# Optimization experiments

Measured on AMD Instinct MI355X. Metric: run time of the kernel, lower is better.

Reference implementation:

```python
import jax, jax.numpy as jnp
import numpy as np

MARGIN = 0.2
ALPHA = 2.0
BETA = 1.5
ANGLE_THRESHOLD = 30.0
EPS_PD = 1e-6   # F.pairwise_distance eps
EPS_CS = 1e-8   # F.cosine_similarity eps
NEG_INF = -1e30
POS_INF = 1e30


def setup_inputs() -> dict:
    key = jax.random.key(0)
    k1, k2, k3 = jax.random.split(key, 3)
    B, F, A = 4096, 512, 3
    features = jax.random.normal(k1, (B, F), dtype=jnp.float32)
    labels = jax.random.randint(k2, (B,), 0, 256)
    angles = jax.random.uniform(k3, (B, A), dtype=jnp.float32) * 90.0  # degrees
    features_orig = jax.random.normal(jax.random.fold_in(key, 7), (B, F), dtype=jnp.float32)
    return {"features": features, "labels": labels, "angles": angles, "features_orig": features_orig}


def _cosine_sim_matrix(f):
    norms = jnp.linalg.norm(f, axis=1)
    denom = jnp.maximum(norms[:, None] * norms[None, :], EPS_CS)
    return (f @ f.T) / denom


def _forward(features, labels, angles, features_orig):
    B = features.shape[0]
    idx = jnp.arange(B)
    # pairwise angle distances [B,B] (torch.cdist p=2)
    adist = jnp.sqrt(jnp.sum((angles[:, None, :] - angles[None, :, :]) ** 2, axis=-1))
    same = labels[:, None] == labels[None, :]
    same = same & ~jnp.eye(B, dtype=bool)          # exclude self
    diff = labels[:, None] != labels[None, :]
    has_pos = same.any(axis=1)
    has_neg = diff.any(axis=1)
    valid = has_pos & has_neg
    # hardest positive: same label, largest angle difference
    pos_idx = jnp.argmax(jnp.where(same, adist, NEG_INF), axis=1)
    # hardest negative: among diff-label within angle threshold, most similar feature;
    # else diff-label with smallest angle difference
    sim = _cosine_sim_matrix(features)
    similar = diff & (adist < ANGLE_THRESHOLD)
    sim_any = similar.any(axis=1)
    neg_idx_hard = jnp.argmax(jnp.where(similar, sim, NEG_INF), axis=1)
    neg_idx_far = jnp.argmin(jnp.where(diff, adist, POS_INF), axis=1)
    neg_idx = jnp.where(sim_any, neg_idx_hard, neg_idx_far)
    # triplet distances (F.pairwise_distance adds eps to the diff)
    a = features
    p = features[pos_idx]
    n = features[neg_idx]
    pos_d = jnp.linalg.norm(a - p + EPS_PD, axis=1)
    neg_d = jnp.linalg.norm(a - n + EPS_PD, axis=1)
    # angle-based weights (non-differentiable, matches .item() in torch)
    pa = adist[idx, pos_idx]
    na = adist[idx, neg_idx]
    w = jnp.where(pa > 45.0, ALPHA, 1.0) * jnp.where(na < 15.0, BETA, 1.0)
    basic = jax.nn.relu(pos_d - neg_d + MARGIN)
    vmask = valid.astype(features.dtype)
    cnt = jnp.maximum(vmask.sum(), 1.0)
    triplet_loss = jnp.sum(w * basic * vmask) / cnt
    # reconstruction term
    num = jnp.sum(features * features_orig, axis=1)
    den = jnp.maximum(jnp.linalg.norm(features, axis=1) * jnp.linalg.norm(features_orig, axis=1), EPS_CS)
    recon = 1.0 - jnp.mean(num / den)
    return triplet_loss + 0.1 * recon


def reference(features, labels, angles, features_orig):
    return _forward(features, labels, angles, features_orig)
```

## Files before the change

### kernel.cpp

```cpp
#include <hip/hip_runtime.h>
#include <math.h>

#define BN 4096
#define FD 512
#define TT 128
#define TJ 64
#define BK 64
#define NJT (BN / TT)
#define NPAIR (NJT * (NJT + 1) / 2)
#define NBLK (NPAIR * 2)
#define NPC 128

typedef __attribute__((ext_vector_type(8))) __bf16 bf16x8;
typedef __attribute__((ext_vector_type(4))) float floatx4;
typedef unsigned long long u64;

__device__ __forceinline__ float wred_sum(float v) {
#pragma unroll
  for (int m = 1; m < 64; m <<= 1) v += __shfl_xor(v, m, 64);
  return v;
}

__device__ __forceinline__ float dot4(float4 a, float4 b) {
  return a.x * b.x + a.y * b.y + a.z * b.z + a.w * b.w;
}

__device__ __forceinline__ unsigned short f2bf(float x) {
  unsigned u = __float_as_uint(x);
  u += 0x7fffu + ((u >> 16) & 1u);
  return (unsigned short)(u >> 16);
}

__device__ __forceinline__ void load16(const void* g, void* l) {
  __builtin_amdgcn_global_load_lds(
      (const __attribute__((address_space(1))) unsigned int*)g,
      (__attribute__((address_space(3))) unsigned int*)l, 16, 0, 0);
}

__device__ __forceinline__ unsigned ford(float v) {
  unsigned u = __float_as_uint(v);
  return u ^ (((unsigned)((int)u >> 31)) | 0x80000000u);
}

template <int N>
__device__ __forceinline__ int rori(int x) {
  return __builtin_amdgcn_update_dpp(0, x, 0x120 | N, 0xf, 0xf, true);
}
template <int N>
__device__ __forceinline__ u64 ror16_u64(u64 k) {
  unsigned lo = (unsigned)rori<N>((int)(unsigned)k);
  unsigned hi = (unsigned)rori<N>((int)(unsigned)(k >> 32));
  return ((u64)hi << 32) | lo;
}
__device__ __forceinline__ u64 red16_max_u64(u64 k) {
  u64 o;
  o = ror16_u64<1>(k); k = o > k ? o : k;
  o = ror16_u64<2>(k); k = o > k ? o : k;
  o = ror16_u64<4>(k); k = o > k ? o : k;
  o = ror16_u64<8>(k); k = o > k ? o : k;
  return k;
}

__device__ __forceinline__ u64 sx64(u64 v, int m) {
  unsigned lo = (unsigned)__shfl_xor((int)(unsigned)v, m, 64);
  unsigned hi = (unsigned)__shfl_xor((int)(unsigned)(v >> 32), m, 64);
  return ((u64)hi << 32) | lo;
}

__global__ __launch_bounds__(256) void k_prep(const float* __restrict__ f,
                                              const float* __restrict__ fo,
                                              const float* __restrict__ angles,
                                              unsigned short* __restrict__ gb,
                                              float* __restrict__ rowr,
                                              float* __restrict__ ax,
                                              float* __restrict__ ay,
                                              float* __restrict__ az) {
  const int i = blockIdx.x * 4 + (threadIdx.x >> 6);
  const int lane = threadIdx.x & 63;
  const int t = blockIdx.x * 256 + threadIdx.x;
  if (t < BN) {
    ax[t] = angles[t * 3 + 0];
    ay[t] = angles[t * 3 + 1];
    az[t] = angles[t * 3 + 2];
  }
  const float4* fr = (const float4*)(f + (size_t)i * FD);
  const float4* orr = (const float4*)(fo + (size_t)i * FD);
  float4 x0 = fr[lane], x1 = fr[lane + 64];
  float4 y0 = orr[lane], y1 = orr[lane + 64];
  float sff = dot4(x0, x0) + dot4(x1, x1);
  float sfo = dot4(x0, y0) + dot4(x1, y1);
  float soo = dot4(y0, y0) + dot4(y1, y1);
  sff = wred_sum(sff);
  sfo = wred_sum(sfo);
  soo = wred_sum(soo);
  float nf = sqrtf(sff);
  float inv = 1.0f / nf;
  ushort4* gr = (ushort4*)(gb + (size_t)i * FD);
  ushort4 s0, s1;
  s0.x = f2bf(x0.x * inv); s0.y = f2bf(x0.y * inv);
  s0.z = f2bf(x0.z * inv); s0.w = f2bf(x0.w * inv);
  s1.x = f2bf(x1.x * inv); s1.y = f2bf(x1.y * inv);
  s1.z = f2bf(x1.z * inv); s1.w = f2bf(x1.w * inv);
  gr[lane] = s0;
  gr[lane + 64] = s1;
  if (lane == 0) {
    rowr[i] = sfo / fmaxf(nf * sqrtf(soo), 1e-8f);
  }
}

__global__ __launch_bounds__(256, 4) void k_sim(const unsigned short* __restrict__ gb,
                                                const int* __restrict__ labels,
                                                const float* __restrict__ ax,
                                                const float* __restrict__ ay,
                                                const float* __restrict__ az,
                                                u64* __restrict__ pkey) {
  __shared__ unsigned short As[TT * BK];
  __shared__ unsigned short Bs[TJ * BK];
  const int h = blockIdx.x & 1;
  int a = 0, rem = blockIdx.x >> 1;
#pragma unroll 1
  while (rem >= NJT - a) { rem -= NJT - a; a++; }
  const int b = a + rem;
  const int i0 = a * TT;
  const int j0 = b * TT + h * TJ;

  const int tid = threadIdx.x;
  const int w = tid >> 6;
  const int lane = tid & 63;

  floatx4 acc[2][4];
#pragma unroll
  for (int u = 0; u < 2; u++)
#pragma unroll
    for (int v = 0; v < 4; v++) acc[u][v] = (floatx4){0.f, 0.f, 0.f, 0.f};

  const int rp = tid >> 3;
  const int q8 = ((tid & 7) ^ (rp & 7)) * 8;
  const unsigned short* gA[4];
  const unsigned short* gB[2];
  unsigned short* lA[4];
  unsigned short* lB[2];
#pragma unroll
  for (int c = 0; c < 4; c++) {
    gA[c] = gb + (size_t)(i0 + rp + 32 * c) * FD + q8;
    lA[c] = As + (tid + 256 * c) * 8;
  }
#pragma unroll
  for (int c = 0; c < 2; c++) {
    gB[c] = gb + (size_t)(j0 + rp + 32 * c) * FD + q8;
    lB[c] = Bs + (tid + 256 * c) * 8;
  }

  const int m = lane & 15;
  const int arow = w * 32 + m;
  const int brow = m;
  const int g4 = lane >> 4;
  const int l7 = lane & 7;
  const int koff0 = (g4 ^ l7) * 8;
  const int koff1 = ((4 + g4) ^ l7) * 8;

  for (int kc = 0; kc < FD; kc += BK) {
#pragma unroll
    for (int c = 0; c < 4; c++) load16(gA[c] + kc, lA[c]);
#pragma unroll
    for (int c = 0; c < 2; c++) load16(gB[c] + kc, lB[c]);
    __syncthreads();
    bf16x8 af[2], bf[4];
#pragma unroll
    for (int u = 0; u < 2; u++)
      af[u] = *(const bf16x8*)(As + (arow + u * 16) * BK + koff0);
#pragma unroll
    for (int v = 0; v < 4; v++)
      bf[v] = *(const bf16x8*)(Bs + (brow + v * 16) * BK + koff0);
#pragma unroll
    for (int u = 0; u < 2; u++)
#pragma unroll
      for (int v = 0; v < 4; v++)
        acc[u][v] = __builtin_amdgcn_mfma_f32_16x16x32_bf16(af[u], bf[v], acc[u][v], 0, 0, 0);
#pragma unroll
    for (int u = 0; u < 2; u++)
      af[u] = *(const bf16x8*)(As + (arow + u * 16) * BK + koff1);
#pragma unroll
    for (int v = 0; v < 4; v++)
      bf[v] = *(const bf16x8*)(Bs + (brow + v * 16) * BK + koff1);
#pragma unroll
    for (int u = 0; u < 2; u++)
#pragma unroll
      for (int v = 0; v < 4; v++)
        acc[u][v] = __builtin_amdgcn_mfma_f32_16x16x32_bf16(af[u], bf[v], acc[u][v], 0, 0, 0);
    __syncthreads();
  }

  const int quad = lane >> 4;
  const int cx = lane & 15;
  int jc[4], lj[4];
  float jx[4], jy[4], jz[4];
#pragma unroll
  for (int v = 0; v < 4; v++) {
    jc[v] = j0 + v * 16 + cx;
    lj[v] = labels[jc[v]];
    jx[v] = ax[jc[v]];
    jy[v] = ay[jc[v]];
    jz[v] = az[jc[v]];
  }
  const size_t rbase = (size_t)(64 + 2 * b + h) * BN;
  u64 ckey[4] = {0, 0, 0, 0};
#pragma unroll
  for (int u = 0; u < 2; u++) {
#pragma unroll
    for (int reg = 0; reg < 4; reg++) {
      int i = i0 + w * 32 + u * 16 + quad * 4 + reg;
      int li = labels[i];
      float a0 = ax[i], a1 = ay[i], a2 = az[i];
      u64 rkey = 0;
      unsigned ni = (unsigned)(~i);
#pragma unroll
      for (int v = 0; v < 4; v++) {
        float d0 = a0 - jx[v];
        float d1 = a1 - jy[v];
        float d2 = a2 - jz[v];
        float dd = d0 * d0 + d1 * d1 + d2 * d2;
        bool ok = (li != lj[v]) && (dd < 900.0f);
        u64 vh = (u64)ford(acc[u][v][reg]) << 32;
        u64 candR = vh | (unsigned)(~jc[v]);
        if (ok && candR > rkey) rkey = candR;
        u64 candC = vh | ni;
        if (ok && candC > ckey[v]) ckey[v] = candC;
      }
      rkey = red16_max_u64(rkey);
      if (cx == 0) pkey[rbase + i] = rkey;
    }
  }
  if (a != b) {
    const size_t cbase = (size_t)(4 * a + w) * BN;
#pragma unroll
    for (int v = 0; v < 4; v++) {
      u64 k = ckey[v];
      u64 o = sx64(k, 16); if (o > k) k = o;
      o = sx64(k, 32); if (o > k) k = o;
      if (quad == 0) pkey[cbase + jc[v]] = k;
    }
  }
}

__global__ __launch_bounds__(256) void k_final(const float* __restrict__ f,
                                               const int* __restrict__ labels,
                                               const float* __restrict__ ax,
                                               const float* __restrict__ ay,
                                               const float* __restrict__ az,
                                               const u64* __restrict__ pkey,
                                               float* __restrict__ rowc,
                                               float* __restrict__ rowv) {
  const int i = blockIdx.x * 4 + (threadIdx.x >> 6);
  const int lane = threadIdx.x & 63;
  const int li = labels[i];
  const float a0 = ax[i], a1 = ay[i], a2 = az[i];

  u64 keyP = 0;
  u64 keyN = ~0ull;
  const float4* ax4 = (const float4*)ax;
  const float4* ay4 = (const float4*)ay;
  const float4* az4 = (const float4*)az;
  const int4* lb4 = (const int4*)labels;
#pragma unroll
  for (int it = 0; it < 16; it++) {
    int bb = it * 64 + lane;
    float4 X = ax4[bb], Y = ay4[bb], Z = az4[bb];
    int4 L = lb4[bb];
    int jb = bb * 4;
#pragma unroll
    for (int s = 0; s < 4; s++) {
      float xx = s == 0 ? X.x : s == 1 ? X.y : s == 2 ? X.z : X.w;
      float yy = s == 0 ? Y.x : s == 1 ? Y.y : s == 2 ? Y.z : Y.w;
      float zz = s == 0 ? Z.x : s == 1 ? Z.y : s == 2 ? Z.z : Z.w;
      int ll = s == 0 ? L.x : s == 1 ? L.y : s == 2 ? L.z : L.w;
      int j = jb + s;
      float d0 = a0 - xx, d1 = a1 - yy, d2 = a2 - zz;
      float dd = d0 * d0 + d1 * d1 + d2 * d2;
      if (ll == li) {
        u64 kp = ((u64)__float_as_uint(dd) << 32) | (unsigned)(~j);
        if (j != i && kp > keyP) keyP = kp;
      } else {
        u64 kn = ((u64)__float_as_uint(dd) << 32) | (unsigned)j;
        if (kn < keyN) keyN = kn;
      }
    }
  }
  const int t = i >> 7;
  u64 s0 = (lane < 4 * t) ? pkey[(size_t)lane * BN + i] : 0;
  u64 s1 = (lane >= 2 * t) ? pkey[(size_t)(64 + lane) * BN + i] : 0;
  u64 keyS = s0 > s1 ? s0 : s1;
#pragma unroll
  for (int off = 1; off < 64; off <<= 1) {
    u64 o = sx64(keyP, off);
    if (o > keyP) keyP = o;
    o = sx64(keyN, off);
    if (o < keyN) keyN = o;
    o = sx64(keyS, off);
    if (o > keyS) keyS = o;
  }
  bool hp = keyP != 0;
  bool hn = keyN != ~0ull;
  if (!(hp && hn)) {
    if (lane == 0) { rowc[i] = 0.0f; rowv[i] = 0.0f; }
    return;
  }
  bool sim_any = keyS != 0;
  int pos = (int)(~(unsigned)keyP);
  int neg = sim_any ? (int)(~(unsigned)keyS) : (int)(unsigned)keyN;

  const float4* fa = (const float4*)(f + (size_t)i * FD);
  const float4* fp = (const float4*)(f + (size_t)pos * FD);
  const float4* fn = (const float4*)(f + (size_t)neg * FD);
  float sp = 0.0f, sn = 0.0f;
#pragma unroll
  for (int t2 = 0; t2 < 2; t2++) {
    float4 xa = fa[lane + t2 * 64];
    float4 xp = fp[lane + t2 * 64];
    float4 xn = fn[lane + t2 * 64];
    float dp;
    dp = xa.x - xp.x + 1e-6f; sp += dp * dp;
    dp = xa.y - xp.y + 1e-6f; sp += dp * dp;
    dp = xa.z - xp.z + 1e-6f; sp += dp * dp;
    dp = xa.w - xp.w + 1e-6f; sp += dp * dp;
    dp = xa.x - xn.x + 1e-6f; sn += dp * dp;
    dp = xa.y - xn.y + 1e-6f; sn += dp * dp;
    dp = xa.z - xn.z + 1e-6f; sn += dp * dp;
    dp = xa.w - xn.w + 1e-6f; sn += dp * dp;
  }
  sp = wred_sum(sp);
  sn = wred_sum(sn);

  if (lane == 0) {
    float pos_d = sqrtf(sp);
    float neg_d = sqrtf(sn);
    float pa = sqrtf(__uint_as_float((unsigned)(keyP >> 32)));
    float n0 = a0 - ax[neg];
    float n1 = a1 - ay[neg];
    float n2 = a2 - az[neg];
    float na = sqrtf(n0 * n0 + n1 * n1 + n2 * n2);
    float w = (pa > 45.0f ? 2.0f : 1.0f) * (na < 15.0f ? 1.5f : 1.0f);
    float basic = fmaxf(pos_d - neg_d + 0.2f, 0.0f);
    rowc[i] = w * basic;
    rowv[i] = 1.0f;
  }
}

__global__ __launch_bounds__(1024) void k_out(const float* __restrict__ rowc,
                                              const float* __restrict__ rowv,
                                              const float* __restrict__ rowr,
                                              float* __restrict__ out) {
  __shared__ float sc[16], sv[16], sr[16];
  const int t = threadIdx.x;
  float c = 0.0f, v = 0.0f, r = 0.0f;
  for (int i = t; i < BN; i += 1024) {
    c += rowc[i];
    v += rowv[i];
    r += rowr[i];
  }
  c = wred_sum(c);
  v = wred_sum(v);
  r = wred_sum(r);
  const int wid = t >> 6;
  if ((t & 63) == 0) { sc[wid] = c; sv[wid] = v; sr[wid] = r; }
  __syncthreads();
  if (t == 0) {
    float C = 0.0f, V = 0.0f, R = 0.0f;
#pragma unroll
    for (int k = 0; k < 16; k++) { C += sc[k]; V += sv[k]; R += sr[k]; }
    float tri = C / fmaxf(V, 1.0f);
    float recon = 1.0f - R / (float)BN;
    out[0] = tri + 0.1f * recon;
  }
}

extern "C" void kernel_launch(void* const* d_in, const int* in_sizes, int n_in,
                              void* d_out, int out_size, void* d_ws, size_t ws_size,
                              hipStream_t stream) {
  const float* feat = (const float*)d_in[0];
  const int* labels = (const int*)d_in[1];
  const float* angles = (const float*)d_in[2];
  const float* forig = (const float*)d_in[3];
  float* out = (float*)d_out;

  char* ws = (char*)d_ws;
  unsigned short* gb = (unsigned short*)ws;
  size_t off = (size_t)BN * FD * sizeof(unsigned short);
  u64* pkey = (u64*)(ws + off);     off += (size_t)NPC * BN * 8;
  float* rowc = (float*)(ws + off); off += (size_t)BN * 4;
  float* rowv = (float*)(ws + off); off += (size_t)BN * 4;
  float* rowr = (float*)(ws + off); off += (size_t)BN * 4;
  float* ax = (float*)(ws + off);   off += (size_t)BN * 4;
  float* ay = (float*)(ws + off);   off += (size_t)BN * 4;
  float* az = (float*)(ws + off);   off += (size_t)BN * 4;

  k_prep<<<BN / 4, 256, 0, stream>>>(feat, forig, angles, gb, rowr, ax, ay, az);
  k_sim<<<NBLK, 256, 0, stream>>>(gb, labels, ax, ay, az, pkey);
  k_final<<<BN / 4, 256, 0, stream>>>(feat, labels, ax, ay, az, pkey, rowc, rowv);
  k_out<<<1, 1024, 0, stream>>>(rowc, rowv, rowr, out);
}
```

Measured before the change: 108.9 us.

## Fuse final reduction into k_final via atomics and remap k_sim block order

Result: slower. 129.3 us (+18.7%).

```diff
diff --git a/kernel.cpp b/kernel.cpp
--- a/kernel.cpp
+++ b/kernel.cpp
@@ -74,7 +74,15 @@
                                               float* __restrict__ rowr,
                                               float* __restrict__ ax,
                                               float* __restrict__ ay,
-                                              float* __restrict__ az) {
+                                              float* __restrict__ az,
+                                              float* __restrict__ acc,
+                                              unsigned* __restrict__ tick) {
+  if (blockIdx.x == 0 && threadIdx.x == 0) {
+    acc[0] = 0.0f;
+    acc[32] = 0.0f;
+    acc[64] = 0.0f;
+    tick[0] = 0u;
+  }
   const int i = blockIdx.x * 4 + (threadIdx.x >> 6);
   const int lane = threadIdx.x & 63;
   const int t = blockIdx.x * 256 + threadIdx.x;
@@ -116,8 +124,10 @@
                                                 u64* __restrict__ pkey) {
   __shared__ unsigned short As[TT * BK];
   __shared__ unsigned short Bs[TJ * BK];
-  const int h = blockIdx.x & 1;
-  int a = 0, rem = blockIdx.x >> 1;
+
+  const int bid = (blockIdx.x & 7) * (NBLK / 8) + (blockIdx.x >> 3);
+  const int h = bid & 1;
+  int a = 0, rem = bid >> 1;
 #pragma unroll 1
   while (rem >= NJT - a) { rem -= NJT - a; a++; }
   const int b = a + rem;
@@ -249,9 +259,12 @@
                                                const float* __restrict__ ay,
                                                const float* __restrict__ az,
                                                const u64* __restrict__ pkey,
-                                               float* __restrict__ rowc,
-                                               float* __restrict__ rowv) {
-  const int i = blockIdx.x * 4 + (threadIdx.x >> 6);
+                                               const float* __restrict__ rowr,
+                                               float* __restrict__ acc,
+                                               unsigned* __restrict__ tick,
+                                               float* __restrict__ out) {
+  const int wv = threadIdx.x >> 6;
+  const int i = blockIdx.x * 4 + wv;
   const int lane = threadIdx.x & 63;
   const int li = labels[i];
   const float a0 = ax[i], a1 = ay[i], a2 = az[i];
@@ -301,76 +314,72 @@
   }
   bool hp = keyP != 0;
   bool hn = keyN != ~0ull;
-  if (!(hp && hn)) {
-    if (lane == 0) { rowc[i] = 0.0f; rowv[i] = 0.0f; }
-    return;
-  }
-  bool sim_any = keyS != 0;
-  int pos = (int)(~(unsigned)keyP);
-  int neg = sim_any ? (int)(~(unsigned)keyS) : (int)(unsigned)keyN;
-
-  const float4* fa = (const float4*)(f + (size_t)i * FD);
-  const float4* fp = (const float4*)(f + (size_t)pos * FD);
-  const float4* fn = (const float4*)(f + (size_t)neg * FD);
-  float sp = 0.0f, sn = 0.0f;
-#pragma unroll
-  for (int t2 = 0; t2 < 2; t2++) {
-    float4 xa = fa[lane + t2 * 64];
-    float4 xp = fp[lane + t2 * 64];
-    float4 xn = fn[lane + t2 * 64];
-    float dp;
-    dp = xa.x - xp.x + 1e-6f; sp += dp * dp;
-    dp = xa.y - xp.y + 1e-6f; sp += dp * dp;
-    dp = xa.z - xp.z + 1e-6f; sp += dp * dp;
-    dp = xa.w - xp.w + 1e-6f; sp += dp * dp;
-    dp = xa.x - xn.x + 1e-6f; sn += dp * dp;
-    dp = xa.y - xn.y + 1e-6f; sn += dp * dp;
-    dp = xa.z - xn.z + 1e-6f; sn += dp * dp;
-    dp = xa.w - xn.w + 1e-6f; sn += dp * dp;
-  }
-  sp = wred_sum(sp);
-  sn = wred_sum(sn);
-
+  float ci = 0.0f, vi = 0.0f;
+  if (hp && hn) {
+    bool sim_any = keyS != 0;
+    int pos = (int)(~(unsigned)keyP);
+    int neg = sim_any ? (int)(~(unsigned)keyS) : (int)(unsigned)keyN;
+
+    const float4* fa = (const float4*)(f + (size_t)i * FD);
+    const float4* fp = (const float4*)(f + (size_t)pos * FD);
+    const float4* fn = (const float4*)(f + (size_t)neg * FD);
+    float sp = 0.0f, sn = 0.0f;
+#pragma unroll
+    for (int t2 = 0; t2 < 2; t2++) {
+      float4 xa = fa[lane + t2 * 64];
+      float4 xp = fp[lane + t2 * 64];
+      float4 xn = fn[lane + t2 * 64];
+      float dp;
+      dp = xa.x - xp.x + 1e-6f; sp += dp * dp;
+      dp = xa.y - xp.y + 1e-6f; sp += dp * dp;
+      dp = xa.z - xp.z + 1e-6f; sp += dp * dp;
+      dp = xa.w - xp.w + 1e-6f; sp += dp * dp;
+      dp = xa.x - xn.x + 1e-6f; sn += dp * dp;
+      dp = xa.y - xn.y + 1e-6f; sn += dp * dp;
+      dp = xa.z - xn.z + 1e-6f; sn += dp * dp;
+      dp = xa.w - xn.w + 1e-6f; sn += dp * dp;
+    }
+    sp = wred_sum(sp);
+    sn = wred_sum(sn);
+
+    if (lane == 0) {
+      float pos_d = sqrtf(sp);
+      float neg_d = sqrtf(sn);
+      float pa = sqrtf(__uint_as_float((unsigned)(keyP >> 32)));
+      float n0 = a0 - ax[neg];
+      float n1 = a1 - ay[neg];
+      float n2 = a2 - az[neg];
+      float na = sqrtf(n0 * n0 + n1 * n1 + n2 * n2);
+      float w = (pa > 45.0f ? 2.0f : 1.0f) * (na < 15.0f ? 1.5f : 1.0f);
+      ci = w * fmaxf(pos_d - neg_d + 0.2f, 0.0f);
+      vi = 1.0f;
+    }
+  }
+
+  __shared__ float sc[4], sv[4], sr[4];
   if (lane == 0) {
-    float pos_d = sqrtf(sp);
-    float neg_d = sqrtf(sn);
-    float pa = sqrtf(__uint_as_float((unsigned)(keyP >> 32)));
-    float n0 = a0 - ax[neg];
-    float n1 = a1 - ay[neg];
-    float n2 = a2 - az[neg];
-    float na = sqrtf(n0 * n0 + n1 * n1 + n2 * n2);
-    float w = (pa > 45.0f ? 2.0f : 1.0f) * (na < 15.0f ? 1.5f : 1.0f);
-    float basic = fmaxf(pos_d - neg_d + 0.2f, 0.0f);
-    rowc[i] = w * basic;
-    rowv[i] = 1.0f;
-  }
-}
-
-__global__ __launch_bounds__(1024) void k_out(const float* __restrict__ rowc,
-                                              const float* __restrict__ rowv,
-                                              const float* __restrict__ rowr,
-                                              float* __restrict__ out) {
-  __shared__ float sc[16], sv[16], sr[16];
-  const int t = threadIdx.x;
-  float c = 0.0f, v = 0.0f, r = 0.0f;
-  for (int i = t; i < BN; i += 1024) {
-    c += rowc[i];
-    v += rowv[i];
-    r += rowr[i];
-  }
-  c = wred_sum(c);
-  v = wred_sum(v);
-  r = wred_sum(r);
-  const int wid = t >> 6;
-  if ((t & 63) == 0) { sc[wid] = c; sv[wid] = v; sr[wid] = r; }
+    sc[wv] = ci;
+    sv[wv] = vi;
+    sr[wv] = rowr[i];
+  }
   __syncthreads();
-  if (t == 0) {
-    float C = 0.0f, V = 0.0f, R = 0.0f;
-#pragma unroll
-    for (int k = 0; k < 16; k++) { C += sc[k]; V += sv[k]; R += sr[k]; }
-    float tri = C / fmaxf(V, 1.0f);
-    float recon = 1.0f - R / (float)BN;
-    out[0] = tri + 0.1f * recon;
+  if (threadIdx.x == 0) {
+    float C = sc[0] + sc[1] + sc[2] + sc[3];
+    float V = sv[0] + sv[1] + sv[2] + sv[3];
+    float R = sr[0] + sr[1] + sr[2] + sr[3];
+    atomicAdd(&acc[0], C);
+    atomicAdd(&acc[32], V);
+    atomicAdd(&acc[64], R);
+    __threadfence();
+    unsigned old = atomicAdd(tick, 1u);
+    if (old == (unsigned)(gridDim.x - 1)) {
+      float Ct = atomicAdd(&acc[0], 0.0f);
+      float Vt = atomicAdd(&acc[32], 0.0f);
+      float Rt = atomicAdd(&acc[64], 0.0f);
+      float tri = Ct / fmaxf(Vt, 1.0f);
+      float recon = 1.0f - Rt * (1.0f / (float)BN);
+      out[0] = tri + 0.1f * recon;
+    }
   }
 }
 
@@ -387,15 +396,14 @@
   unsigned short* gb = (unsigned short*)ws;
   size_t off = (size_t)BN * FD * sizeof(unsigned short);
   u64* pkey = (u64*)(ws + off);     off += (size_t)NPC * BN * 8;
-  float* rowc = (float*)(ws + off); off += (size_t)BN * 4;
-  float* rowv = (float*)(ws + off); off += (size_t)BN * 4;
   float* rowr = (float*)(ws + off); off += (size_t)BN * 4;
   float* ax = (float*)(ws + off);   off += (size_t)BN * 4;
   float* ay = (float*)(ws + off);   off += (size_t)BN * 4;
   float* az = (float*)(ws + off);   off += (size_t)BN * 4;
-
-  k_prep<<<BN / 4, 256, 0, stream>>>(feat, forig, angles, gb, rowr, ax, ay, az);
+  float* acc = (float*)(ws + off);  off += 128 * 4;
+  unsigned* tick = (unsigned*)(ws + off); off += 128;
+
+  k_prep<<<BN / 4, 256, 0, stream>>>(feat, forig, angles, gb, rowr, ax, ay, az, acc, tick);
   k_sim<<<NBLK, 256, 0, stream>>>(gb, labels, ax, ay, az, pkey);
-  k_final<<<BN / 4, 256, 0, stream>>>(feat, labels, ax, ay, az, pkey, rowc, rowv);
-  k_out<<<1, 1024, 0, stream>>>(rowc, rowv, rowr, out);
-}
+  k_final<<<BN / 4, 256, 0, stream>>>(feat, labels, ax, ay, az, pkey, rowr, acc, tick, out);
+}
```

## Fuse hardest-positive and nearest-negative search into the similarity tile epilogue

Applied to the files above, without the earlier changes.

New measurement: 142.8 us. 31.1% more time.

```diff
diff --git a/kernel.cpp b/kernel.cpp
--- a/kernel.cpp
+++ b/kernel.cpp
@@ -66,6 +66,8 @@
   unsigned hi = (unsigned)__shfl_xor((int)(unsigned)(v >> 32), m, 64);
   return ((u64)hi << 32) | lo;
 }
+
+__device__ __forceinline__ u64 umax64(u64 a, u64 b) { return a > b ? a : b; }
 
 __global__ __launch_bounds__(256) void k_prep(const float* __restrict__ f,
                                               const float* __restrict__ fo,
@@ -193,6 +195,7 @@
 
   const int quad = lane >> 4;
   const int cx = lane & 15;
+  const size_t CHN = (size_t)NPC * BN;
   int jc[4], lj[4];
   float jx[4], jy[4], jz[4];
 #pragma unroll
@@ -204,7 +207,9 @@
     jz[v] = az[jc[v]];
   }
   const size_t rbase = (size_t)(64 + 2 * b + h) * BN;
-  u64 ckey[4] = {0, 0, 0, 0};
+  u64 ckeyS[4] = {0, 0, 0, 0};
+  u64 ckeyP[4] = {0, 0, 0, 0};
+  u64 ckeyN[4] = {0, 0, 0, 0};
 #pragma unroll
   for (int u = 0; u < 2; u++) {
 #pragma unroll
@@ -212,7 +217,7 @@
       int i = i0 + w * 32 + u * 16 + quad * 4 + reg;
       int li = labels[i];
       float a0 = ax[i], a1 = ay[i], a2 = az[i];
-      u64 rkey = 0;
+      u64 rkeyS = 0, rkeyP = 0, rkeyN = 0;
       unsigned ni = (unsigned)(~i);
 #pragma unroll
       for (int v = 0; v < 4; v++) {
@@ -220,31 +225,53 @@
         float d1 = a1 - jy[v];
         float d2 = a2 - jz[v];
         float dd = d0 * d0 + d1 * d1 + d2 * d2;
-        bool ok = (li != lj[v]) && (dd < 900.0f);
+        unsigned ddb = __float_as_uint(dd);
+        bool dl = (li != lj[v]);
+        bool sl = !dl && (i != jc[v]);
+        bool ok = dl && (dd < 900.0f);
         u64 vh = (u64)ford(acc[u][v][reg]) << 32;
-        u64 candR = vh | (unsigned)(~jc[v]);
-        if (ok && candR > rkey) rkey = candR;
-        u64 candC = vh | ni;
-        if (ok && candC > ckey[v]) ckey[v] = candC;
+        u64 cSR = vh | (unsigned)(~jc[v]);
+        if (ok && cSR > rkeyS) rkeyS = cSR;
+        u64 cSC = vh | ni;
+        if (ok && cSC > ckeyS[v]) ckeyS[v] = cSC;
+        u64 ddh = (u64)ddb << 32;
+        u64 cPR = ddh | (unsigned)(~jc[v]);
+        if (sl && cPR > rkeyP) rkeyP = cPR;
+        u64 cPC = ddh | ni;
+        if (sl && cPC > ckeyP[v]) ckeyP[v] = cPC;
+        u64 cNR = ~(ddh | (unsigned)jc[v]);
+        if (dl && cNR > rkeyN) rkeyN = cNR;
+        u64 cNC = ~(ddh | (unsigned)i);
+        if (dl && cNC > ckeyN[v]) ckeyN[v] = cNC;
       }
-      rkey = red16_max_u64(rkey);
-      if (cx == 0) pkey[rbase + i] = rkey;
+      rkeyS = red16_max_u64(rkeyS);
+      rkeyP = red16_max_u64(rkeyP);
+      rkeyN = red16_max_u64(rkeyN);
+      if (cx == 0) {
+        pkey[rbase + i] = rkeyS;
+        pkey[CHN + rbase + i] = rkeyP;
+        pkey[2 * CHN + rbase + i] = rkeyN;
+      }
     }
   }
   if (a != b) {
     const size_t cbase = (size_t)(4 * a + w) * BN;
 #pragma unroll
     for (int v = 0; v < 4; v++) {
-      u64 k = ckey[v];
-      u64 o = sx64(k, 16); if (o > k) k = o;
-      o = sx64(k, 32); if (o > k) k = o;
-      if (quad == 0) pkey[cbase + jc[v]] = k;
+      u64 kS = ckeyS[v], kP = ckeyP[v], kN = ckeyN[v];
+      kS = umax64(kS, sx64(kS, 16)); kS = umax64(kS, sx64(kS, 32));
+      kP = umax64(kP, sx64(kP, 16)); kP = umax64(kP, sx64(kP, 32));
+      kN = umax64(kN, sx64(kN, 16)); kN = umax64(kN, sx64(kN, 32));
+      if (quad == 0) {
+        pkey[cbase + jc[v]] = kS;
+        pkey[CHN + cbase + jc[v]] = kP;
+        pkey[2 * CHN + cbase + jc[v]] = kN;
+      }
     }
   }
 }
 
 __global__ __launch_bounds__(256) void k_final(const float* __restrict__ f,
-                                               const int* __restrict__ labels,
                                                const float* __restrict__ ax,
                                                const float* __restrict__ ay,
                                                const float* __restrict__ az,
@@ -253,60 +280,30 @@
                                                float* __restrict__ rowv) {
   const int i = blockIdx.x * 4 + (threadIdx.x >> 6);
   const int lane = threadIdx.x & 63;
-  const int li = labels[i];
-  const float a0 = ax[i], a1 = ay[i], a2 = az[i];
-
-  u64 keyP = 0;
-  u64 keyN = ~0ull;
-  const float4* ax4 = (const float4*)ax;
-  const float4* ay4 = (const float4*)ay;
-  const float4* az4 = (const float4*)az;
-  const int4* lb4 = (const int4*)labels;
-#pragma unroll
-  for (int it = 0; it < 16; it++) {
-    int bb = it * 64 + lane;
-    float4 X = ax4[bb], Y = ay4[bb], Z = az4[bb];
-    int4 L = lb4[bb];
-    int jb = bb * 4;
-#pragma unroll
-    for (int s = 0; s < 4; s++) {
-      float xx = s == 0 ? X.x : s == 1 ? X.y : s == 2 ? X.z : X.w;
-      float yy = s == 0 ? Y.x : s == 1 ? Y.y : s == 2 ? Y.z : Y.w;
-      float zz = s == 0 ? Z.x : s == 1 ? Z.y : s == 2 ? Z.z : Z.w;
-      int ll = s == 0 ? L.x : s == 1 ? L.y : s == 2 ? L.z : L.w;
-      int j = jb + s;
-      float d0 = a0 - xx, d1 = a1 - yy, d2 = a2 - zz;
-      float dd = d0 * d0 + d1 * d1 + d2 * d2;
-      if (ll == li) {
-        u64 kp = ((u64)__float_as_uint(dd) << 32) | (unsigned)(~j);
-        if (j != i && kp > keyP) keyP = kp;
-      } else {
-        u64 kn = ((u64)__float_as_uint(dd) << 32) | (unsigned)j;
-        if (kn < keyN) keyN = kn;
-      }
-    }
-  }
   const int t = i >> 7;
-  u64 s0 = (lane < 4 * t) ? pkey[(size_t)lane * BN + i] : 0;
-  u64 s1 = (lane >= 2 * t) ? pkey[(size_t)(64 + lane) * BN + i] : 0;
-  u64 keyS = s0 > s1 ? s0 : s1;
+  const size_t CHN = (size_t)NPC * BN;
+  const bool c_ok = lane < 4 * t;
+  const bool r_ok = lane >= 2 * t;
+  const size_t coff = (size_t)lane * BN + i;
+  const size_t roff = (size_t)(64 + lane) * BN + i;
+  u64 keyS = umax64(c_ok ? pkey[coff] : 0, r_ok ? pkey[roff] : 0);
+  u64 keyP = umax64(c_ok ? pkey[CHN + coff] : 0, r_ok ? pkey[CHN + roff] : 0);
+  u64 keyNc = umax64(c_ok ? pkey[2 * CHN + coff] : 0, r_ok ? pkey[2 * CHN + roff] : 0);
 #pragma unroll
   for (int off = 1; off < 64; off <<= 1) {
-    u64 o = sx64(keyP, off);
-    if (o > keyP) keyP = o;
-    o = sx64(keyN, off);
-    if (o < keyN) keyN = o;
-    o = sx64(keyS, off);
-    if (o > keyS) keyS = o;
+    u64 o = sx64(keyS, off); if (o > keyS) keyS = o;
+    o = sx64(keyP, off); if (o > keyP) keyP = o;
+    o = sx64(keyNc, off); if (o > keyNc) keyNc = o;
   }
   bool hp = keyP != 0;
-  bool hn = keyN != ~0ull;
+  bool hn = keyNc != 0;
   if (!(hp && hn)) {
     if (lane == 0) { rowc[i] = 0.0f; rowv[i] = 0.0f; }
     return;
   }
   bool sim_any = keyS != 0;
   int pos = (int)(~(unsigned)keyP);
+  u64 keyN = ~keyNc;
   int neg = sim_any ? (int)(~(unsigned)keyS) : (int)(unsigned)keyN;
 
   const float4* fa = (const float4*)(f + (size_t)i * FD);
@@ -335,9 +332,9 @@
     float pos_d = sqrtf(sp);
     float neg_d = sqrtf(sn);
     float pa = sqrtf(__uint_as_float((unsigned)(keyP >> 32)));
-    float n0 = a0 - ax[neg];
-    float n1 = a1 - ay[neg];
-    float n2 = a2 - az[neg];
+    float n0 = ax[i] - ax[neg];
+    float n1 = ay[i] - ay[neg];
+    float n2 = az[i] - az[neg];
     float na = sqrtf(n0 * n0 + n1 * n1 + n2 * n2);
     float w = (pa > 45.0f ? 2.0f : 1.0f) * (na < 15.0f ? 1.5f : 1.0f);
     float basic = fmaxf(pos_d - neg_d + 0.2f, 0.0f);
@@ -386,7 +383,7 @@
   char* ws = (char*)d_ws;
   unsigned short* gb = (unsigned short*)ws;
   size_t off = (size_t)BN * FD * sizeof(unsigned short);
-  u64* pkey = (u64*)(ws + off);     off += (size_t)NPC * BN * 8;
+  u64* pkey = (u64*)(ws + off);     off += (size_t)3 * NPC * BN * 8;
   float* rowc = (float*)(ws + off); off += (size_t)BN * 4;
   float* rowv = (float*)(ws + off); off += (size_t)BN * 4;
   float* rowr = (float*)(ws + off); off += (size_t)BN * 4;
@@ -396,6 +393,6 @@
 
   k_prep<<<BN / 4, 256, 0, stream>>>(feat, forig, angles, gb, rowr, ax, ay, az);
   k_sim<<<NBLK, 256, 0, stream>>>(gb, labels, ax, ay, az, pkey);
-  k_final<<<BN / 4, 256, 0, stream>>>(feat, labels, ax, ay, az, pkey, rowc, rowv);
+  k_final<<<BN / 4, 256, 0, stream>>>(feat, ax, ay, az, pkey, rowc, rowv);
   k_out<<<1, 1024, 0, stream>>>(rowc, rowv, rowr, out);
 }
```

## Move angle-based positive/negative search into extra k_sim blocks and pack angles+labels

Applied to the files above, without the earlier changes.

New measurement: 110.4 us, median of 2. No clear change (+1.3%).

```diff
diff --git a/kernel.cpp b/kernel.cpp
--- a/kernel.cpp
+++ b/kernel.cpp
@@ -10,6 +10,9 @@
 #define NPAIR (NJT * (NJT + 1) / 2)
 #define NBLK (NPAIR * 2)
 #define NPC 128
+#define NJR 32
+#define JR (BN / NJR)
+#define NABLK (NJR * (BN / 256))
 
 typedef __attribute__((ext_vector_type(8))) __bf16 bf16x8;
 typedef __attribute__((ext_vector_type(4))) float floatx4;
@@ -67,21 +70,25 @@
   return ((u64)hi << 32) | lo;
 }
 
+__device__ __forceinline__ u64 umax64(u64 a, u64 b) { return a > b ? a : b; }
+
 __global__ __launch_bounds__(256) void k_prep(const float* __restrict__ f,
                                               const float* __restrict__ fo,
                                               const float* __restrict__ angles,
+                                              const int* __restrict__ labels,
                                               unsigned short* __restrict__ gb,
                                               float* __restrict__ rowr,
-                                              float* __restrict__ ax,
-                                              float* __restrict__ ay,
-                                              float* __restrict__ az) {
+                                              float4* __restrict__ apk) {
   const int i = blockIdx.x * 4 + (threadIdx.x >> 6);
   const int lane = threadIdx.x & 63;
   const int t = blockIdx.x * 256 + threadIdx.x;
   if (t < BN) {
-    ax[t] = angles[t * 3 + 0];
-    ay[t] = angles[t * 3 + 1];
-    az[t] = angles[t * 3 + 2];
+    float4 q;
+    q.x = angles[t * 3 + 0];
+    q.y = angles[t * 3 + 1];
+    q.z = angles[t * 3 + 2];
+    q.w = __uint_as_float((unsigned)labels[t]);
+    apk[t] = q;
   }
   const float4* fr = (const float4*)(f + (size_t)i * FD);
   const float4* orr = (const float4*)(fo + (size_t)i * FD);
@@ -109,13 +116,46 @@
 }
 
 __global__ __launch_bounds__(256, 4) void k_sim(const unsigned short* __restrict__ gb,
-                                                const int* __restrict__ labels,
-                                                const float* __restrict__ ax,
-                                                const float* __restrict__ ay,
-                                                const float* __restrict__ az,
-                                                u64* __restrict__ pkey) {
-  __shared__ unsigned short As[TT * BK];
+                                                const float4* __restrict__ apk,
+                                                u64* __restrict__ pkey,
+                                                u64* __restrict__ pangP,
+                                                u64* __restrict__ pangN) {
+  __shared__ __align__(16) unsigned short As[TT * BK];
   __shared__ unsigned short Bs[TJ * BK];
+  const int tid = threadIdx.x;
+
+  if (blockIdx.x >= NBLK) {
+    const int q = blockIdx.x - NBLK;
+    const int jr = q & (NJR - 1);
+    const int ib = q >> 5;
+    const int i = ib * 256 + tid;
+    float4* aj = (float4*)As;
+    if (tid < JR) aj[tid] = apk[jr * JR + tid];
+    __syncthreads();
+    float4 me = apk[i];
+    const unsigned lib = __float_as_uint(me.w);
+    const int j0 = jr * JR;
+    u64 keyP = 0, keyNc = 0;
+#pragma unroll 4
+    for (int jj = 0; jj < JR; jj++) {
+      float4 aw = aj[jj];
+      int j = j0 + jj;
+      float d0 = me.x - aw.x;
+      float d1 = me.y - aw.y;
+      float d2 = me.z - aw.z;
+      float dd = d0 * d0 + d1 * d1 + d2 * d2;
+      u64 ddh = (u64)__float_as_uint(dd) << 32;
+      bool same = (__float_as_uint(aw.w) == lib);
+      u64 kp = ddh | (unsigned)(~j);
+      if (same && j != i && kp > keyP) keyP = kp;
+      u64 kn = ~(ddh | (unsigned)j);
+      if (!same && kn > keyNc) keyNc = kn;
+    }
+    pangP[(size_t)jr * BN + i] = keyP;
+    pangN[(size_t)jr * BN + i] = keyNc;
+    return;
+  }
+
   const int h = blockIdx.x & 1;
   int a = 0, rem = blockIdx.x >> 1;
 #pragma unroll 1
@@ -124,7 +164,6 @@
   const int i0 = a * TT;
   const int j0 = b * TT + h * TJ;
 
-  const int tid = threadIdx.x;
   const int w = tid >> 6;
   const int lane = tid & 63;
 
@@ -193,15 +232,17 @@
 
   const int quad = lane >> 4;
   const int cx = lane & 15;
-  int jc[4], lj[4];
+  int jc[4];
+  unsigned ljb[4];
   float jx[4], jy[4], jz[4];
 #pragma unroll
   for (int v = 0; v < 4; v++) {
     jc[v] = j0 + v * 16 + cx;
-    lj[v] = labels[jc[v]];
-    jx[v] = ax[jc[v]];
-    jy[v] = ay[jc[v]];
-    jz[v] = az[jc[v]];
+    float4 qj = apk[jc[v]];
+    jx[v] = qj.x;
+    jy[v] = qj.y;
+    jz[v] = qj.z;
+    ljb[v] = __float_as_uint(qj.w);
   }
   const size_t rbase = (size_t)(64 + 2 * b + h) * BN;
   u64 ckey[4] = {0, 0, 0, 0};
@@ -210,17 +251,17 @@
 #pragma unroll
     for (int reg = 0; reg < 4; reg++) {
       int i = i0 + w * 32 + u * 16 + quad * 4 + reg;
-      int li = labels[i];
-      float a0 = ax[i], a1 = ay[i], a2 = az[i];
+      float4 qi = apk[i];
+      unsigned lib = __float_as_uint(qi.w);
       u64 rkey = 0;
       unsigned ni = (unsigned)(~i);
 #pragma unroll
       for (int v = 0; v < 4; v++) {
-        float d0 = a0 - jx[v];
-        float d1 = a1 - jy[v];
-        float d2 = a2 - jz[v];
+        float d0 = qi.x - jx[v];
+        float d1 = qi.y - jy[v];
+        float d2 = qi.z - jz[v];
         float dd = d0 * d0 + d1 * d1 + d2 * d2;
-        bool ok = (li != lj[v]) && (dd < 900.0f);
+        bool ok = (lib != ljb[v]) && (dd < 900.0f);
         u64 vh = (u64)ford(acc[u][v][reg]) << 32;
         u64 candR = vh | (unsigned)(~jc[v]);
         if (ok && candR > rkey) rkey = candR;
@@ -244,69 +285,36 @@
 }
 
 __global__ __launch_bounds__(256) void k_final(const float* __restrict__ f,
-                                               const int* __restrict__ labels,
-                                               const float* __restrict__ ax,
-                                               const float* __restrict__ ay,
-                                               const float* __restrict__ az,
+                                               const float4* __restrict__ apk,
                                                const u64* __restrict__ pkey,
+                                               const u64* __restrict__ pangP,
+                                               const u64* __restrict__ pangN,
                                                float* __restrict__ rowc,
                                                float* __restrict__ rowv) {
   const int i = blockIdx.x * 4 + (threadIdx.x >> 6);
   const int lane = threadIdx.x & 63;
-  const int li = labels[i];
-  const float a0 = ax[i], a1 = ay[i], a2 = az[i];
-
-  u64 keyP = 0;
-  u64 keyN = ~0ull;
-  const float4* ax4 = (const float4*)ax;
-  const float4* ay4 = (const float4*)ay;
-  const float4* az4 = (const float4*)az;
-  const int4* lb4 = (const int4*)labels;
-#pragma unroll
-  for (int it = 0; it < 16; it++) {
-    int bb = it * 64 + lane;
-    float4 X = ax4[bb], Y = ay4[bb], Z = az4[bb];
-    int4 L = lb4[bb];
-    int jb = bb * 4;
-#pragma unroll
-    for (int s = 0; s < 4; s++) {
-      float xx = s == 0 ? X.x : s == 1 ? X.y : s == 2 ? X.z : X.w;
-      float yy = s == 0 ? Y.x : s == 1 ? Y.y : s == 2 ? Y.z : Y.w;
-      float zz = s == 0 ? Z.x : s == 1 ? Z.y : s == 2 ? Z.z : Z.w;
-      int ll = s == 0 ? L.x : s == 1 ? L.y : s == 2 ? L.z : L.w;
-      int j = jb + s;
-      float d0 = a0 - xx, d1 = a1 - yy, d2 = a2 - zz;
-      float dd = d0 * d0 + d1 * d1 + d2 * d2;
-      if (ll == li) {
-        u64 kp = ((u64)__float_as_uint(dd) << 32) | (unsigned)(~j);
-        if (j != i && kp > keyP) keyP = kp;
-      } else {
-        u64 kn = ((u64)__float_as_uint(dd) << 32) | (unsigned)j;
-        if (kn < keyN) keyN = kn;
-      }
-    }
-  }
   const int t = i >> 7;
+
   u64 s0 = (lane < 4 * t) ? pkey[(size_t)lane * BN + i] : 0;
   u64 s1 = (lane >= 2 * t) ? pkey[(size_t)(64 + lane) * BN + i] : 0;
-  u64 keyS = s0 > s1 ? s0 : s1;
+  u64 keyS = umax64(s0, s1);
+  u64 keyP = (lane < NJR) ? pangP[(size_t)lane * BN + i] : 0;
+  u64 keyNc = (lane >= NJR) ? pangN[(size_t)(lane - NJR) * BN + i] : 0;
 #pragma unroll
   for (int off = 1; off < 64; off <<= 1) {
-    u64 o = sx64(keyP, off);
-    if (o > keyP) keyP = o;
-    o = sx64(keyN, off);
-    if (o < keyN) keyN = o;
-    o = sx64(keyS, off);
-    if (o > keyS) keyS = o;
+    u64 o = sx64(keyS, off); if (o > keyS) keyS = o;
+    o = sx64(keyP, off); if (o > keyP) keyP = o;
+    o = sx64(keyNc, off); if (o > keyNc) keyNc = o;
   }
   bool hp = keyP != 0;
-  bool hn = keyN != ~0ull;
+  bool hn = keyNc != 0;
   if (!(hp && hn)) {
     if (lane == 0) { rowc[i] = 0.0f; rowv[i] = 0.0f; }
     return;
   }
   bool sim_any = keyS != 0;
   int pos = (int)(~(unsigned)keyP);
+  u64 keyN = ~keyNc;
   int neg = sim_any ? (int)(~(unsigned)keyS) : (int)(unsigned)keyN;
 
   const float4* fa = (const float4*)(f + (size_t)i * FD);
@@ -332,12 +340,14 @@
   sn = wred_sum(sn);
 
   if (lane == 0) {
+    float4 qi = apk[i];
+    float4 qn = apk[neg];
     float pos_d = sqrtf(sp);
     float neg_d = sqrtf(sn);
     float pa = sqrtf(__uint_as_float((unsigned)(keyP >> 32)));
-    float n0 = a0 - ax[neg];
-    float n1 = a1 - ay[neg];
-    float n2 = a2 - az[neg];
+    float n0 = qi.x - qn.x;
+    float n1 = qi.y - qn.y;
+    float n2 = qi.z - qn.z;
     float na = sqrtf(n0 * n0 + n1 * n1 + n2 * n2);
     float w = (pa > 45.0f ? 2.0f : 1.0f) * (na < 15.0f ? 1.5f : 1.0f);
     float basic = fmaxf(pos_d - neg_d + 0.2f, 0.0f);
@@ -386,16 +396,16 @@
   char* ws = (char*)d_ws;
   unsigned short* gb = (unsigned short*)ws;
   size_t off = (size_t)BN * FD * sizeof(unsigned short);
-  u64* pkey = (u64*)(ws + off);     off += (size_t)NPC * BN * 8;
-  float* rowc = (float*)(ws + off); off += (size_t)BN * 4;
-  float* rowv = (float*)(ws + off); off += (size_t)BN * 4;
-  float* rowr = (float*)(ws + off); off += (size_t)BN * 4;
-  float* ax = (float*)(ws + off);   off += (size_t)BN * 4;
-  float* ay = (float*)(ws + off);   off += (size_t)BN * 4;
-  float* az = (float*)(ws + off);   off += (size_t)BN * 4;
-
-  k_prep<<<BN / 4, 256, 0, stream>>>(feat, forig, angles, gb, rowr, ax, ay, az);
-  k_sim<<<NBLK, 256, 0, stream>>>(gb, labels, ax, ay, az, pkey);
-  k_final<<<BN / 4, 256, 0, stream>>>(feat, labels, ax, ay, az, pkey, rowc, rowv);
+  u64* pkey = (u64*)(ws + off);      off += (size_t)NPC * BN * 8;
+  u64* pangP = (u64*)(ws + off);     off += (size_t)NJR * BN * 8;
+  u64* pangN = (u64*)(ws + off);     off += (size_t)NJR * BN * 8;
+  float4* apk = (float4*)(ws + off); off += (size_t)BN * 16;
+  float* rowc = (float*)(ws + off);  off += (size_t)BN * 4;
+  float* rowv = (float*)(ws + off);  off += (size_t)BN * 4;
+  float* rowr = (float*)(ws + off);  off += (size_t)BN * 4;
+
+  k_prep<<<BN / 4, 256, 0, stream>>>(feat, forig, angles, labels, gb, rowr, apk);
+  k_sim<<<NBLK + NABLK, 256, 0, stream>>>(gb, apk, pkey, pangP, pangN);
+  k_final<<<BN / 4, 256, 0, stream>>>(feat, apk, pkey, pangP, pangN, rowc, rowv);
   k_out<<<1, 1024, 0, stream>>>(rowc, rowv, rowr, out);
 }
```
